# Kernel optimization log

Hardware: AMD Instinct MI355X
Metric: run time of the kernel (lower is better)

## Reference

```python
import jax, jax.numpy as jnp
import numpy as np

B, Q, M = 4, 256, 256
QS, KS, H = 512, 512, 512


def setup_inputs() -> dict:
    key = jax.random.key(0)
    ks = jax.random.split(key, 12)
    s = 0.02
    return {
        "query": jax.random.normal(ks[0], (B, Q, QS), dtype=jnp.float32),
        "memory": jax.random.normal(ks[1], (B, M, KS), dtype=jnp.float32),
        "mask": jax.random.randint(ks[2], (B, M), 0, 2).astype(jnp.bool_),
        "Wk": jax.random.normal(ks[3], (H, KS), dtype=jnp.float32) * s,
        "bk": jnp.zeros((H,), dtype=jnp.float32),
        "Wq": jax.random.normal(ks[4], (H, QS), dtype=jnp.float32) * s,
        "bq": jnp.zeros((H,), dtype=jnp.float32),
        "Wl": jax.random.normal(ks[5], (1, H), dtype=jnp.float32) * s,
        "bl": jnp.zeros((1,), dtype=jnp.float32),
        "Wo": jax.random.normal(ks[6], (QS, QS + KS), dtype=jnp.float32) * s,
        "bo": jnp.zeros((QS,), dtype=jnp.float32),
    }


def reference(query, memory, mask, Wk, bk, Wq, bq, Wl, bl, Wo, bo):
    # Projections: q [B,Q,H], k [B,M,H]
    q = jnp.einsum("bqd,hd->bqh", query, Wq) + bq
    k = jnp.einsum("bmd,hd->bmh", memory, Wk) + bk
    # Additive (Bahdanau) scores: broadcast add -> tanh -> hidden->1 projection
    e = jnp.tanh(q[:, :, None, :] + k[:, None, :, :])  # [B,Q,M,H]
    logits = jnp.einsum("bqmh,h->bqm", e, Wl[0]) + bl[0]  # [B,Q,M]
    logits = jnp.where(mask[:, None, :], jnp.float32(-1e18), logits)
    weights = jax.nn.softmax(logits, axis=-1)  # [B,Q,M]
    attns = jnp.einsum("bqm,bmd->bqd", weights, memory)  # [B,Q,KS]
    combined = jnp.concatenate([query, attns], axis=-1)  # [B,Q,QS+KS]
    output = jnp.tanh(jnp.einsum("bqc,oc->bqo", combined, Wo) + bo)
    return output, weights
```

## Files before the change

kernel.cpp:

```cpp
#include <hip/hip_runtime.h>


#define B_   4
#define Q_   256
#define M_   256
#define H_   512
#define QS_  512
#define KS_  512

#define TSC 2.8853900817779268f

typedef __attribute__((ext_vector_type(8))) short bf16x8;
typedef __attribute__((ext_vector_type(4))) float f32x4;

__device__ __forceinline__ float fast_exp2(float x) { return __builtin_amdgcn_exp2f(x); }

__device__ __forceinline__ float tanh_fast(float x) {
    float e = fast_exp2(x * TSC);
    return 1.0f - 2.0f * __builtin_amdgcn_rcpf(e + 1.0f);
}

__device__ __forceinline__ unsigned short rne_bf16(float f) {
    unsigned b = __builtin_bit_cast(unsigned, f);
    return (unsigned short)((b + 0x7FFFu + ((b >> 16) & 1u)) >> 16);
}

__device__ __forceinline__ float bf2f(unsigned short u) {
    return __builtin_bit_cast(float, (unsigned)u << 16);
}

__device__ __forceinline__ bf16x8 cvt8(const float* __restrict__ p) {
    const float4 lo = *(const float4*)p;
    const float4 hi = *(const float4*)(p + 4);
    float f[8] = {lo.x, lo.y, lo.z, lo.w, hi.x, hi.y, hi.z, hi.w};
    union { bf16x8 v; unsigned short u[8]; } r;
#pragma unroll
    for (int j = 0; j < 8; ++j) r.u[j] = rne_bf16(f[j]);
    return r.v;
}

__global__ __launch_bounds__(256) void prep(const float* __restrict__ query,
                                            const float* __restrict__ memory,
                                            const float* __restrict__ Wq,
                                            const float* __restrict__ Wk,
                                            const float* __restrict__ Wo,
                                            const unsigned char* __restrict__ mask,
                                            unsigned short* __restrict__ qbf,
                                            unsigned short* __restrict__ mbf,
                                            unsigned short* __restrict__ wqbf,
                                            unsigned short* __restrict__ wkbf,
                                            unsigned short* __restrict__ wobf,
                                            int* __restrict__ maskN, int nmask) {
    if (blockIdx.x == 1024) {
        __shared__ int flags[4];
        const int tid = threadIdx.x;
        int any = 0;
        for (int i = tid; i < nmask; i += 256)
            if ((i & 3) && mask[i]) any = 1;
        int wany = __any(any);
        if ((tid & 63) == 0) flags[tid >> 6] = wany ? 1 : 0;
        __syncthreads();
        const int isbool = flags[0] | flags[1] | flags[2] | flags[3];
        const int* ri = (const int*)mask;
        for (int i = tid; i < nmask; i += 256)
            maskN[i] = isbool ? (int)mask[i] : ri[i];
        return;
    }
    const int u = blockIdx.x * 256 + threadIdx.x;
    const float* src;
    unsigned short* dst;
    int off;
    if (u < 131072) {
        if (u < 65536) { src = query;  dst = qbf; off = u; }
        else           { src = memory; dst = mbf; off = u - 65536; }
    } else if (u < 196608) {
        if (u < 163840) { src = Wq; dst = wqbf; off = u - 131072; }
        else            { src = Wk; dst = wkbf; off = u - 163840; }
    } else { src = Wo; dst = wobf; off = u - 196608; }
    const int i = off * 8;
    *(bf16x8*)&dst[i] = cvt8(&src[i]);
}

__global__ __launch_bounds__(256) void gemm5(const unsigned short* __restrict__ qbf,
                                             const unsigned short* __restrict__ mbf,
                                             const unsigned short* __restrict__ wqbf,
                                             const unsigned short* __restrict__ wkbf,
                                             const unsigned short* __restrict__ wobf,
                                             const float* __restrict__ bq,
                                             const float* __restrict__ bk,
                                             const float* __restrict__ bo,
                                             unsigned short* __restrict__ Eqb,
                                             unsigned short* __restrict__ Ekb,
                                             float* __restrict__ Y1,
                                             unsigned short* __restrict__ Zb) {
    const int lane = threadIdx.x & 63;
    const int wid  = threadIdx.x >> 6;
    const int gt  = blockIdx.x * 4 + wid;
    const int seg = gt >> 9;
    const int t   = gt & 511;
    const int tm  = t >> 4;
    const int tn  = t & 15;

    const unsigned short* A;
    const unsigned short* W;
    const float* bias;
    int ldW, wko;
    if (seg == 0)      { A = qbf; W = wqbf; ldW = 512;  wko = 0;   bias = bq; }
    else if (seg == 1) { A = mbf; W = wkbf; ldW = 512;  wko = 0;   bias = bk; }
    else if (seg == 2) { A = qbf; W = wobf; ldW = 1024; wko = 0;   bias = bo; }
    else               { A = mbf; W = wobf; ldW = 1024; wko = 512; bias = nullptr; }

    const int rA = tm * 32 + (lane & 15);
    const int rB = tn * 32 + (lane & 15);
    const int ko = (lane >> 4) * 8;

    f32x4 acc00 = {0,0,0,0}, acc01 = {0,0,0,0}, acc10 = {0,0,0,0}, acc11 = {0,0,0,0};
#pragma unroll
    for (int kt = 0; kt < 512; kt += 32) {
        bf16x8 a0 = *(const bf16x8*)&A[rA * 512 + kt + ko];
        bf16x8 a1 = *(const bf16x8*)&A[(rA + 16) * 512 + kt + ko];
        bf16x8 b0 = *(const bf16x8*)&W[rB * ldW + wko + kt + ko];
        bf16x8 b1 = *(const bf16x8*)&W[(rB + 16) * ldW + wko + kt + ko];
        acc00 = __builtin_amdgcn_mfma_f32_16x16x32_bf16(a0, b0, acc00, 0, 0, 0);
        acc01 = __builtin_amdgcn_mfma_f32_16x16x32_bf16(a0, b1, acc01, 0, 0, 0);
        acc10 = __builtin_amdgcn_mfma_f32_16x16x32_bf16(a1, b0, acc10, 0, 0, 0);
        acc11 = __builtin_amdgcn_mfma_f32_16x16x32_bf16(a1, b1, acc11, 0, 0, 0);
    }
    const int col = tn * 32 + (lane & 15);
    const int r0  = tm * 32 + (lane >> 4) * 4;
    const float bv0 = bias ? bias[col] : 0.f;
    const float bv1 = bias ? bias[col + 16] : 0.f;
    if (seg < 2) {
        unsigned short* E = (seg == 0) ? Eqb : Ekb;
#pragma unroll
        for (int j = 0; j < 4; ++j) {
            E[(r0 + j) * 512 + col]           = rne_bf16(fast_exp2(TSC * (acc00[j] + bv0)));
            E[(r0 + j) * 512 + col + 16]      = rne_bf16(fast_exp2(TSC * (acc01[j] + bv1)));
            E[(r0 + 16 + j) * 512 + col]      = rne_bf16(fast_exp2(TSC * (acc10[j] + bv0)));
            E[(r0 + 16 + j) * 512 + col + 16] = rne_bf16(fast_exp2(TSC * (acc11[j] + bv1)));
        }
    } else if (seg == 2) {
#pragma unroll
        for (int j = 0; j < 4; ++j) {
            Y1[(r0 + j) * 512 + col]           = acc00[j] + bv0;
            Y1[(r0 + j) * 512 + col + 16]      = acc01[j] + bv1;
            Y1[(r0 + 16 + j) * 512 + col]      = acc10[j] + bv0;
            Y1[(r0 + 16 + j) * 512 + col + 16] = acc11[j] + bv1;
        }
    } else {
#pragma unroll
        for (int j = 0; j < 4; ++j) {
            Zb[(r0 + j) * 512 + col]           = rne_bf16(acc00[j]);
            Zb[(r0 + j) * 512 + col + 16]      = rne_bf16(acc01[j]);
            Zb[(r0 + 16 + j) * 512 + col]      = rne_bf16(acc10[j]);
            Zb[(r0 + 16 + j) * 512 + col + 16] = rne_bf16(acc11[j]);
        }
    }
}

__global__ __launch_bounds__(1024) void attn_fused(const int* __restrict__ maskN,
                                                   const unsigned short* __restrict__ Eqb,
                                                   const unsigned short* __restrict__ Ekb,
                                                   const float* __restrict__ Wl,
                                                   const float* __restrict__ bl,
                                                   const float* __restrict__ Y1,
                                                   const unsigned short* __restrict__ Zb,
                                                   float* __restrict__ wout,
                                                   float* __restrict__ out) {
    const int b = blockIdx.y;
    const int q0 = blockIdx.x * 4;
    const int tid = threadIdx.x;
    const int wid = tid >> 6;
    const int lane = tid & 63;

    __shared__ float slog[4][M_];
    __shared__ float swt[4][M_];
    __shared__ int s_list[M_];
    __shared__ int s_base[4];
    __shared__ int s_cnt;
    __shared__ int s_allmask;

    int msk_ = 1, prefix_ = 0;
    if (tid < 256) {
        msk_ = maskN[(b << 8) + tid];
        unsigned long long vote = __ballot(msk_ == 0);
        prefix_ = __popcll(vote & ((1ull << lane) - 1ull));
        if (lane == 0) s_base[wid] = __popcll(vote);
    }
    __syncthreads();
    if (tid == 0) {
        int s = 0;
#pragma unroll
        for (int i = 0; i < 4; ++i) { int c = s_base[i]; s_base[i] = s; s += c; }
        s_cnt = s;
    }
    __syncthreads();
    if (tid < 256 && !msk_) s_list[s_base[wid] + prefix_] = tid;

    float qreg[4][8], wlr[8];
#pragma unroll
    for (int qi = 0; qi < 4; ++qi) {
        union { bf16x8 v; unsigned short u[8]; } qv;
        qv.v = *(const bf16x8*)&Eqb[((b << 8) + (q0 + qi)) * H_ + lane * 8];
#pragma unroll
        for (int h = 0; h < 8; ++h) qreg[qi][h] = bf2f(qv.u[h]);
    }
    *(float4*)&wlr[0] = *(const float4*)&Wl[lane * 8];
    *(float4*)&wlr[4] = *(const float4*)&Wl[lane * 8 + 4];
    const float bl0 = bl[0];

    float sumWL = wlr[0] + wlr[1] + wlr[2] + wlr[3] + wlr[4] + wlr[5] + wlr[6] + wlr[7];
#pragma unroll
    for (int off = 32; off; off >>= 1) sumWL += __shfl_xor(sumWL, off, 64);

    __syncthreads();
    const int cnt = s_cnt;

    for (int idx = wid; idx < cnt; idx += 16) {
        const int m = s_list[idx];
        union { bf16x8 v; unsigned short u[8]; } kv;
        kv.v = *(const bf16x8*)&Ekb[((b << 8) + m) * H_ + lane * 8];
        float acc[4] = {0.f, 0.f, 0.f, 0.f};
#pragma unroll
        for (int h = 0; h < 8; ++h) {
            const float ek = bf2f(kv.u[h]);
            const float wv = wlr[h];
#pragma unroll
            for (int qi = 0; qi < 4; ++qi) {
                const float e = qreg[qi][h] * ek;
                const float r = __builtin_amdgcn_rcpf(e + 1.0f);
                acc[qi] = fmaf(wv, r, acc[qi]);
            }
        }
#pragma unroll
        for (int qi = 0; qi < 4; ++qi) {
            float v = acc[qi];
#pragma unroll
            for (int off = 32; off; off >>= 1) v += __shfl_xor(v, off, 64);
            if (lane == 0) slog[qi][m] = sumWL - 2.0f * v + bl0;
        }
    }
    __syncthreads();

    if (wid < 4) {
        const int qi = wid;
        float x[4];
        int mk[4];
#pragma unroll
        for (int j = 0; j < 4; ++j) {
            const int m = lane * 4 + j;
            mk[j] = maskN[(b << 8) + m];
            x[j] = mk[j] ? -1e30f : slog[qi][m];
        }
        float mx = fmaxf(fmaxf(x[0], x[1]), fmaxf(x[2], x[3]));
#pragma unroll
        for (int off = 32; off; off >>= 1) mx = fmaxf(mx, __shfl_xor(mx, off, 64));
        float e[4], s = 0.f;
#pragma unroll
        for (int j = 0; j < 4; ++j) {
            e[j] = mk[j] ? 0.f : fast_exp2((x[j] - mx) * 1.4426950408889634f);
            s += e[j];
        }
#pragma unroll
        for (int off = 32; off; off >>= 1) s += __shfl_xor(s, off, 64);
        float w4[4];
        if (s > 0.f) {
            const float inv = 1.0f / s;
#pragma unroll
            for (int j = 0; j < 4; ++j) w4[j] = e[j] * inv;
        } else {
#pragma unroll
            for (int j = 0; j < 4; ++j) w4[j] = 1.0f / (float)M_;
        }
#pragma unroll
        for (int j = 0; j < 4; ++j) swt[qi][lane * 4 + j] = w4[j];
        *(float4*)&wout[((b << 8) + (q0 + qi)) * M_ + lane * 4] = *(const float4*)w4;
        if (tid == 0) s_allmask = (s <= 0.f) ? 1 : 0;
    }
    __syncthreads();

    if (tid < QS_) {
        const int am = s_allmask;
        float a[4] = {0.f, 0.f, 0.f, 0.f};
        const unsigned short* Zrow = &Zb[((b << 8)) * QS_ + tid];
        if (!am) {
            for (int idx = 0; idx < cnt; ++idx) {
                const int m = s_list[idx];
                const float zv = bf2f(Zrow[m * QS_]);
#pragma unroll
                for (int qi = 0; qi < 4; ++qi) a[qi] = fmaf(swt[qi][m], zv, a[qi]);
            }
        } else {
            for (int m = 0; m < M_; ++m) {
                const float zv = bf2f(Zrow[m * QS_]);
#pragma unroll
                for (int qi = 0; qi < 4; ++qi) a[qi] = fmaf(swt[qi][m], zv, a[qi]);
            }
        }
#pragma unroll
        for (int qi = 0; qi < 4; ++qi) {
            const int r = (b << 8) + q0 + qi;
            out[r * QS_ + tid] = tanh_fast(Y1[r * QS_ + tid] + a[qi]);
        }
    }
}

extern "C" void kernel_launch(void* const* d_in, const int* in_sizes, int n_in,
                              void* d_out, int out_size, void* d_ws, size_t ws_size,
                              hipStream_t stream) {
    const float* query  = (const float*)d_in[0];
    const float* memory = (const float*)d_in[1];
    const void*  mask   = d_in[2];
    const float* Wk = (const float*)d_in[3];
    const float* bk = (const float*)d_in[4];
    const float* Wq = (const float*)d_in[5];
    const float* bq = (const float*)d_in[6];
    const float* Wl = (const float*)d_in[7];
    const float* bl = (const float*)d_in[8];
    const float* Wo = (const float*)d_in[9];
    const float* bo = (const float*)d_in[10];

    float* out  = (float*)d_out;
    float* wout = out + B_ * Q_ * QS_;

    float* ws = (float*)d_ws;
    float*          Y1    = ws;
    unsigned short* Eqb   = (unsigned short*)(ws + 524288);
    unsigned short* Ekb   = (unsigned short*)(ws + 786432);
    unsigned short* Zb    = (unsigned short*)(ws + 1048576);
    unsigned short* qbf   = (unsigned short*)(ws + 1310720);
    unsigned short* mbf   = (unsigned short*)(ws + 1572864);
    unsigned short* wqbf  = (unsigned short*)(ws + 1835008);
    unsigned short* wkbf  = (unsigned short*)(ws + 1966080);
    unsigned short* wobf  = (unsigned short*)(ws + 2097152);
    int*            maskN = (int*)(ws + 2359296);

    hipLaunchKernelGGL(prep, dim3(1025), dim3(256), 0, stream,
                       query, memory, Wq, Wk, Wo, (const unsigned char*)mask,
                       qbf, mbf, wqbf, wkbf, wobf, maskN, in_sizes[2]);
    hipLaunchKernelGGL(gemm5, dim3(512), dim3(256), 0, stream,
                       qbf, mbf, wqbf, wkbf, wobf, bq, bk, bo, Eqb, Ekb, Y1, Zb);
    hipLaunchKernelGGL(attn_fused, dim3(Q_ / 4, B_), dim3(1024), 0, stream,
                       maskN, Eqb, Ekb, Wl, bl, Y1, Zb, wout, out);
}
```

Before: 55.49 us.

## Fuse fp32-to-bf16 conversion into LDS-tiled projection GEMM, drop prep kernel

Removes the separate prep kernel that converted inputs and weights to bf16 in workspace. The GEMM kernel now reads fp32 directly, converts while staging 64x128 tiles into shared memory, and reuses each tile across four waves in a 64x64 block tile. Mask normalization moves into an extra block of the GEMM launch. This cuts one launch and the bf16 write/read round trip. The cost is repeated conversion work per tile and LDS synchronisation with no double buffering.

```diff
diff --git a/kernel.cpp b/kernel.cpp
--- a/kernel.cpp
+++ b/kernel.cpp
@@ -39,19 +39,22 @@
     return r.v;
 }
 
-__global__ __launch_bounds__(256) void prep(const float* __restrict__ query,
-                                            const float* __restrict__ memory,
-                                            const float* __restrict__ Wq,
-                                            const float* __restrict__ Wk,
-                                            const float* __restrict__ Wo,
-                                            const unsigned char* __restrict__ mask,
-                                            unsigned short* __restrict__ qbf,
-                                            unsigned short* __restrict__ mbf,
-                                            unsigned short* __restrict__ wqbf,
-                                            unsigned short* __restrict__ wkbf,
-                                            unsigned short* __restrict__ wobf,
-                                            int* __restrict__ maskN, int nmask) {
-    if (blockIdx.x == 1024) {
+__global__ __launch_bounds__(256) void gemm5(const float* __restrict__ query,
+                                             const float* __restrict__ memory,
+                                             const float* __restrict__ Wq,
+                                             const float* __restrict__ Wk,
+                                             const float* __restrict__ Wo,
+                                             const float* __restrict__ bq,
+                                             const float* __restrict__ bk,
+                                             const float* __restrict__ bo,
+                                             const unsigned char* __restrict__ mask,
+                                             int nmask,
+                                             unsigned short* __restrict__ Eqb,
+                                             unsigned short* __restrict__ Ekb,
+                                             float* __restrict__ Y1,
+                                             unsigned short* __restrict__ Zb,
+                                             int* __restrict__ maskN) {
+    if (blockIdx.x == 512) {
         __shared__ int flags[4];
         const int tid = threadIdx.x;
         int any = 0;
@@ -66,68 +69,62 @@
             maskN[i] = isbool ? (int)mask[i] : ri[i];
         return;
     }
-    const int u = blockIdx.x * 256 + threadIdx.x;
-    const float* src;
-    unsigned short* dst;
-    int off;
-    if (u < 131072) {
-        if (u < 65536) { src = query;  dst = qbf; off = u; }
-        else           { src = memory; dst = mbf; off = u - 65536; }
-    } else if (u < 196608) {
-        if (u < 163840) { src = Wq; dst = wqbf; off = u - 131072; }
-        else            { src = Wk; dst = wkbf; off = u - 163840; }
-    } else { src = Wo; dst = wobf; off = u - 196608; }
-    const int i = off * 8;
-    *(bf16x8*)&dst[i] = cvt8(&src[i]);
-}
-
-__global__ __launch_bounds__(256) void gemm5(const unsigned short* __restrict__ qbf,
-                                             const unsigned short* __restrict__ mbf,
-                                             const unsigned short* __restrict__ wqbf,
-                                             const unsigned short* __restrict__ wkbf,
-                                             const unsigned short* __restrict__ wobf,
-                                             const float* __restrict__ bq,
-                                             const float* __restrict__ bk,
-                                             const float* __restrict__ bo,
-                                             unsigned short* __restrict__ Eqb,
-                                             unsigned short* __restrict__ Ekb,
-                                             float* __restrict__ Y1,
-                                             unsigned short* __restrict__ Zb) {
-    const int lane = threadIdx.x & 63;
-    const int wid  = threadIdx.x >> 6;
-    const int gt  = blockIdx.x * 4 + wid;
-    const int seg = gt >> 9;
-    const int t   = gt & 511;
-    const int tm  = t >> 4;
-    const int tn  = t & 15;
-
-    const unsigned short* A;
-    const unsigned short* W;
+
+    __shared__ unsigned short As[64][136];
+    __shared__ unsigned short Ws[64][136];
+
+    const int tid  = threadIdx.x;
+    const int lane = tid & 63;
+    const int wid  = tid >> 6;
+    const int seg  = blockIdx.x >> 7;
+    const int sb   = blockIdx.x & 127;
+    const int bm   = sb >> 3;
+    const int bn   = sb & 7;
+
+    const float* A;
+    const float* W;
     const float* bias;
     int ldW, wko;
-    if (seg == 0)      { A = qbf; W = wqbf; ldW = 512;  wko = 0;   bias = bq; }
-    else if (seg == 1) { A = mbf; W = wkbf; ldW = 512;  wko = 0;   bias = bk; }
-    else if (seg == 2) { A = qbf; W = wobf; ldW = 1024; wko = 0;   bias = bo; }
-    else               { A = mbf; W = wobf; ldW = 1024; wko = 512; bias = nullptr; }
-
-    const int rA = tm * 32 + (lane & 15);
-    const int rB = tn * 32 + (lane & 15);
-    const int ko = (lane >> 4) * 8;
+    if (seg == 0)      { A = query;  W = Wq; ldW = 512;  wko = 0;   bias = bq; }
+    else if (seg == 1) { A = memory; W = Wk; ldW = 512;  wko = 0;   bias = bk; }
+    else if (seg == 2) { A = query;  W = Wo; ldW = 1024; wko = 0;   bias = bo; }
+    else               { A = memory; W = Wo; ldW = 1024; wko = 512; bias = nullptr; }
+
+    const int wr = wid >> 1;
+    const int wc = wid & 1;
+    const int lr = tid >> 2;
+    const int lq = tid & 3;
+
+    const float* Arow = &A[(bm * 64 + lr) * 512];
+    const float* Wrow = &W[(bn * 64 + lr) * ldW + wko];
 
     f32x4 acc00 = {0,0,0,0}, acc01 = {0,0,0,0}, acc10 = {0,0,0,0}, acc11 = {0,0,0,0};
-#pragma unroll
-    for (int kt = 0; kt < 512; kt += 32) {
-        bf16x8 a0 = *(const bf16x8*)&A[rA * 512 + kt + ko];
-        bf16x8 a1 = *(const bf16x8*)&A[(rA + 16) * 512 + kt + ko];
-        bf16x8 b0 = *(const bf16x8*)&W[rB * ldW + wko + kt + ko];
-        bf16x8 b1 = *(const bf16x8*)&W[(rB + 16) * ldW + wko + kt + ko];
-        acc00 = __builtin_amdgcn_mfma_f32_16x16x32_bf16(a0, b0, acc00, 0, 0, 0);
-        acc01 = __builtin_amdgcn_mfma_f32_16x16x32_bf16(a0, b1, acc01, 0, 0, 0);
-        acc10 = __builtin_amdgcn_mfma_f32_16x16x32_bf16(a1, b0, acc10, 0, 0, 0);
-        acc11 = __builtin_amdgcn_mfma_f32_16x16x32_bf16(a1, b1, acc11, 0, 0, 0);
-    }
-    const int col = tn * 32 + (lane & 15);
-    const int r0  = tm * 32 + (lane >> 4) * 4;
+
+    for (int kt = 0; kt < 512; kt += 128) {
+#pragma unroll
+        for (int j = 0; j < 4; ++j) {
+            const int c8 = (lq + 4 * j) * 8;
+            *(bf16x8*)&As[lr][c8] = cvt8(&Arow[kt + c8]);
+            *(bf16x8*)&Ws[lr][c8] = cvt8(&Wrow[kt + c8]);
+        }
+        __syncthreads();
+#pragma unroll
+        for (int ks = 0; ks < 4; ++ks) {
+            const int kk = ks * 32 + (lane >> 4) * 8;
+            bf16x8 a0 = *(const bf16x8*)&As[wr * 32 + (lane & 15)][kk];
+            bf16x8 a1 = *(const bf16x8*)&As[wr * 32 + 16 + (lane & 15)][kk];
+            bf16x8 b0 = *(const bf16x8*)&Ws[wc * 32 + (lane & 15)][kk];
+            bf16x8 b1 = *(const bf16x8*)&Ws[wc * 32 + 16 + (lane & 15)][kk];
+            acc00 = __builtin_amdgcn_mfma_f32_16x16x32_bf16(a0, b0, acc00, 0, 0, 0);
+            acc01 = __builtin_amdgcn_mfma_f32_16x16x32_bf16(a0, b1, acc01, 0, 0, 0);
+            acc10 = __builtin_amdgcn_mfma_f32_16x16x32_bf16(a1, b0, acc10, 0, 0, 0);
+            acc11 = __builtin_amdgcn_mfma_f32_16x16x32_bf16(a1, b1, acc11, 0, 0, 0);
+        }
+        __syncthreads();
+    }
+
+    const int col = bn * 64 + wc * 32 + (lane & 15);
+    const int r0  = bm * 64 + wr * 32 + (lane >> 4) * 4;
     const float bv0 = bias ? bias[col] : 0.f;
     const float bv1 = bias ? bias[col + 16] : 0.f;
     if (seg < 2) {
@@ -328,18 +325,12 @@
     unsigned short* Eqb   = (unsigned short*)(ws + 524288);
     unsigned short* Ekb   = (unsigned short*)(ws + 786432);
     unsigned short* Zb    = (unsigned short*)(ws + 1048576);
-    unsigned short* qbf   = (unsigned short*)(ws + 1310720);
-    unsigned short* mbf   = (unsigned short*)(ws + 1572864);
-    unsigned short* wqbf  = (unsigned short*)(ws + 1835008);
-    unsigned short* wkbf  = (unsigned short*)(ws + 1966080);
-    unsigned short* wobf  = (unsigned short*)(ws + 2097152);
-    int*            maskN = (int*)(ws + 2359296);
-
-    hipLaunchKernelGGL(prep, dim3(1025), dim3(256), 0, stream,
-                       query, memory, Wq, Wk, Wo, (const unsigned char*)mask,
-                       qbf, mbf, wqbf, wkbf, wobf, maskN, in_sizes[2]);
-    hipLaunchKernelGGL(gemm5, dim3(512), dim3(256), 0, stream,
-                       qbf, mbf, wqbf, wkbf, wobf, bq, bk, bo, Eqb, Ekb, Y1, Zb);
+    int*            maskN = (int*)(ws + 1310720);
+
+    hipLaunchKernelGGL(gemm5, dim3(513), dim3(256), 0, stream,
+                       query, memory, Wq, Wk, Wo, bq, bk, bo,
+                       (const unsigned char*)mask, in_sizes[2],
+                       Eqb, Ekb, Y1, Zb, maskN);
     hipLaunchKernelGGL(attn_fused, dim3(Q_ / 4, B_), dim3(1024), 0, stream,
                        maskN, Eqb, Ekb, Wl, bl, Y1, Zb, wout, out);
 }
```

Result: faster. 47.91 us (median of 2 runs) (-13.7%).
